# Kernel optimization log

Measured on AMD Instinct MI355X. Metric: run time of the kernel, lower is better.

## Reference

```python
import jax, jax.numpy as jnp
import numpy as np

EPS = 1e-5
N_HEADS = 32
TEMPERATURE = 1.0


def _inorm(x, g, b):
    # InstanceNorm2d (affine): normalize over H,W per (N, C)
    m = jnp.mean(x, axis=(-2, -1), keepdims=True)
    v = jnp.var(x, axis=(-2, -1), keepdims=True)
    return (x - m) * jax.lax.rsqrt(v + EPS) * g + b


def _resample(x, out_hw):
    # Fourier (spectral) resampling, matching neuraloperator's resample for skips
    H, W = x.shape[-2:]
    Ho, Wo = out_hw
    if (H, W) == (Ho, Wo):
        return x
    xf = jnp.fft.rfft2(x, norm='forward')
    kh = min(H, Ho) // 2
    kw = min(W // 2 + 1, Wo // 2 + 1)
    of = jnp.zeros(x.shape[:-2] + (Ho, Wo // 2 + 1), dtype=xf.dtype)
    of = of.at[..., :kh, :kw].set(xf[..., :kh, :kw])
    of = of.at[..., -kh:, :kw].set(xf[..., -kh:, :kw])
    return jnp.fft.irfft2(of, s=(Ho, Wo), norm='forward')


def _spec_conv(x, w, out_hw):
    # w: [2(pos/neg rows), in, out, m1, m2, 2(re/im)]; fft_norm='forward'
    m1, m2 = w.shape[3], w.shape[4]
    Ho, Wo = out_hw
    wc = w[..., 0] + 1j * w[..., 1]  # [2, in, out, m1, m2]
    xf = jnp.fft.rfft2(x, norm='forward')  # [B, Cin, H, W//2+1]
    top = jnp.einsum('bimn,iomn->bomn', xf[:, :, :m1, :m2], wc[0])
    bot = jnp.einsum('bimn,iomn->bomn', xf[:, :, -m1:, :m2], wc[1])
    of = jnp.zeros((x.shape[0], w.shape[2], Ho, Wo // 2 + 1), dtype=xf.dtype)
    of = of.at[:, :, :m1, :m2].set(top)
    of = of.at[:, :, -m1:, :m2].set(bot)
    return jnp.fft.irfft2(of, s=(Ho, Wo), norm='forward')


def _fno_layer(x, w, ws, bs, out_hw, norm_gb=None, act=False):
    # one FNOBlock layer: spectral conv + linear (1x1) skip, optional instance norm + gelu
    skip = jnp.einsum('bchw,oc->bohw', x, ws) + bs[None, :, None, None]
    skip = _resample(skip, out_hw)
    fno = _spec_conv(x, w, out_hw)
    if norm_gb is not None:
        fno = _inorm(fno, norm_gb[0], norm_gb[1])
    y = fno + skip
    if act:
        y = jax.nn.gelu(y, approximate=False)  # torch F.gelu default = exact erf
    return y


def _forward(x, wK, wKs, bKs, wQ, wQs, bQs, wV, wVs, bVs, wP, wPs, bPs,
             wM0, wM0s, bM0s, wM1, wM1s, bM1s, norm_g, norm_b):
    B, T, H, W = x.shape  # token_codimension == 1 -> tokens T == channels
    xa = x.reshape(B * T, 1, H, W)
    xa_n = _inorm(xa, norm_g[0], norm_b[0])  # self.norm1
    # K, Q at half resolution (output_scaling_factor = 1/scale, scale = 2); V at full res
    k = _fno_layer(xa_n, wK, wKs, bKs, (H // 2, W // 2))
    q = _fno_layer(xa_n, wQ, wQs, bQs, (H // 2, W // 2))
    v = _fno_layer(xa_n, wV, wVs, bVs, (H, W))

    def to_seq(z):
        h, w = z.shape[-2:]
        z = z.reshape(B, T, N_HEADS, 1, h, w).transpose(0, 2, 1, 3, 4, 5)
        return z.reshape(B, N_HEADS, T, h * w)  # d = head_codim = 1

    qs, ks, vs = to_seq(q), to_seq(k), to_seq(v)
    scores = jnp.einsum('bhtd,bhsd->bhts', qs, ks) / (np.sqrt(ks.shape[-1]).astype(np.float32) * TEMPERATURE)
    attn_w = jax.nn.softmax(scores, axis=-1)
    out = jnp.einsum('bhts,bhsd->bhtd', attn_w, vs)  # [B, heads, T, H*W]
    out = out.reshape(B, N_HEADS, T, 1, H, W).transpose(0, 2, 1, 3, 4, 5)
    out = out.reshape(B * T, N_HEADS, H, W)
    # proj: n_heads*head_codim != token_codim -> FNO projection back to 1 channel
    projd = _fno_layer(out, wP, wPs, bPs, (H, W))
    attention = _inorm(projd + xa, norm_g[1], norm_b[1])  # attention_normalizer
    an = _inorm(attention, norm_g[2], norm_b[2])  # self.norm2
    # permutation-equivariant mixer: 2 FNO layers, instance_norm, gelu between layers
    m = _fno_layer(an, wM0, wM0s, bM0s, (H, W), (norm_g[3], norm_b[3]), act=True)
    m = _fno_layer(m, wM1, wM1s, bM1s, (H, W), (norm_g[4], norm_b[4]), act=False)
    output = _inorm(m, norm_g[5], norm_b[5]) + attention  # mixer_out_normalizer + residual
    return output.reshape(B, T, H, W)


def setup_inputs() -> dict:
    key = jax.random.key(0)
    ks = jax.random.split(key, 16)
    B, T, H, W, heads = 2, 32, 128, 128, 32

    def rn(k, shape, s=1.0):
        return jax.random.normal(k, shape, jnp.float32) * s

    inp = {'x': rn(ks[0], (B, T, H, W))}
    for i, nm in enumerate(['K', 'Q', 'V']):
        inp['w' + nm] = rn(ks[1 + 3 * i], (2, 1, heads, 16, 16, 2), 1.0 / heads)
        inp['w' + nm + 's'] = rn(ks[2 + 3 * i], (heads, 1), 1.0)
        inp['b' + nm + 's'] = jnp.zeros((heads,), jnp.float32)
    inp['wP'] = rn(ks[10], (2, heads, 1, 32, 32, 2), 1.0 / heads)
    inp['wPs'] = rn(ks[11], (1, heads), 1.0 / heads)
    inp['bPs'] = jnp.zeros((1,), jnp.float32)
    inp['wM0'] = rn(ks[12], (2, 1, 1, 32, 32, 2), 1.0)
    inp['wM0s'] = rn(ks[13], (1, 1), 1.0)
    inp['bM0s'] = jnp.zeros((1,), jnp.float32)
    inp['wM1'] = rn(ks[14], (2, 1, 1, 32, 32, 2), 1.0)
    inp['wM1s'] = rn(ks[15], (1, 1), 1.0)
    inp['bM1s'] = jnp.zeros((1,), jnp.float32)
    inp['norm_g'] = jnp.ones((6,), jnp.float32)
    inp['norm_b'] = jnp.zeros((6,), jnp.float32)
    return inp


def reference(x, wK, wKs, bKs, wQ, wQs, bQs, wV, wVs, bVs, wP, wPs, bPs,
              wM0, wM0s, bM0s, wM1, wM1s, bM1s, norm_g, norm_b):
    return _forward(x, wK, wKs, bKs, wQ, wQs, bQs, wV, wVs, bVs, wP, wPs, bPs,
                    wM0, wM0s, bM0s, wM1, wM1s, bM1s, norm_g, norm_b)
```

## Files before the change

### kernel.cpp

```cpp
#include <hip/hip_runtime.h>
#include <math.h>


#define EPSV 1e-5f
#define PI2 6.283185307179586f

typedef float2 cf;

__device__ __forceinline__ cf cmul(cf a, cf b){ return make_float2(a.x*b.x - a.y*b.y, a.x*b.y + a.y*b.x); }
__device__ __forceinline__ cf ldc(const float* p){ return make_float2(p[0], p[1]); }
__device__ __forceinline__ void stc(float* p, cf v){ p[0]=v.x; p[1]=v.y; }

__device__ __forceinline__ void init_tw(cf* tw, int N, float dir){
  for (int j = threadIdx.x; j < N; j += blockDim.x){
    float s, c; sincosf(dir * PI2 * (float)j / (float)N, &s, &c);
    tw[j] = make_float2(c, s);
  }
}

__device__ void breduce2(float& a, float& b){
  __shared__ float sha[16], shb[16];
  for (int off = 32; off > 0; off >>= 1){
    a += __shfl_down(a, off, 64);
    b += __shfl_down(b, off, 64);
  }
  int w = threadIdx.x >> 6, lane = threadIdx.x & 63;
  int nw = (blockDim.x + 63) >> 6;
  if (lane == 0){ sha[w] = a; shb[w] = b; }
  __syncthreads();
  if (threadIdx.x == 0){
    for (int i = 1; i < nw; ++i){ a += sha[i]; b += shb[i]; }
    sha[0] = a; shb[0] = b;
  }
  __syncthreads();
  a = sha[0]; b = shb[0];
  __syncthreads();
}

__device__ __forceinline__ cf kq_mode(const float* w, int o, int kh, int kw){
  if (kw < 16){
    if (kh < 16)  return ldc(w + ((o*16+kh)*16+kw)*2);
    if (kh >= 48) return ldc(w + (((32+o)*16+(kh-48))*16+kw)*2);
  }
  return make_float2(0.f,0.f);
}

__global__ __launch_bounds__(256) void k_gamma_xstats(
                      const float* __restrict__ wQ, const float* __restrict__ wQs,
                      const float* __restrict__ bQs,
                      const float* __restrict__ wK, const float* __restrict__ wKs,
                      const float* __restrict__ bKs,
                      const float* __restrict__ x, const float* __restrict__ ng,
                      const float* __restrict__ nb,
                      float* __restrict__ gam, float* __restrict__ gcons,
                      float* __restrict__ stats, float* __restrict__ normAB){
  if (blockIdx.x >= 32){
    int n = blockIdx.x - 32;
    const float* im = x + n*16384;
    float s=0.f, s2=0.f;
    for (int i=threadIdx.x;i<16384;i+=256){ float v=im[i]; s+=v; s2=fmaf(v,v,s2); }
    breduce2(s,s2);
    if (threadIdx.x==0){
      float m = s*(1.f/16384.f), var = s2*(1.f/16384.f)-m*m;
      float A = rsqrtf(var+EPSV)*ng[0];
      normAB[n*2]=A; normAB[n*2+1]=nb[0]-m*A;
    }
    return;
  }
  int o = blockIdx.x;
  if (o==0){ for (int i=threadIdx.x;i<640;i+=256) stats[i]=0.f; }
  float sQ=wQs[o], sK=wKs[o];
  for (int m = threadIdx.x; m < 2112; m += 256){
    int kh = m/33, kw = m-kh*33;
    cf g;
    if (kw == 0){
      int mh = (64-kh)&63;
      cf qp = kq_mode(wQ,o,kh,0);  qp.x += sQ;
      cf qm = kq_mode(wQ,o,mh,0);  qm.x += sQ;
      cf qt = make_float2(0.5f*(qp.x+qm.x), 0.5f*(qp.y-qm.y));
      cf kp = kq_mode(wK,o,kh,0);  kp.x += sK;
      cf km = kq_mode(wK,o,mh,0);  km.x += sK;
      cf kt = make_float2(0.5f*(kp.x+km.x), 0.5f*(kp.y-km.y));
      g = make_float2(64.f*(qt.x*kt.x + qt.y*kt.y), 64.f*(qt.y*kt.x - qt.x*kt.y));
    } else if (kw == 32){
      g = make_float2(64.f*sQ*sK, 0.f);
    } else {
      cf q = kq_mode(wQ,o,kh,kw); q.x += sQ;
      cf k = kq_mode(wK,o,kh,kw); k.x += sK;
      g = make_float2(128.f*(q.x*k.x + q.y*k.y), 128.f*(q.y*k.x - q.x*k.y));
    }
    stc(gam + (o*2112+m)*2, g);
  }
  if (threadIdx.x == 0){
    float qt0 = sQ + kq_mode(wQ,o,0,0).x;
    float kt0 = sK + kq_mode(wK,o,0,0).x;
    gcons[o]    = 64.f*bKs[o]*qt0;
    gcons[32+o] = 64.f*bQs[o]*kt0;
    gcons[64+o] = 64.f*bQs[o]*bKs[o];
  }
}

__global__ __launch_bounds__(1024) void k_fwd2d(const float* __restrict__ x, const float* __restrict__ normAB,
                                                float* __restrict__ F){
  __shared__ float zb[16384];
  __shared__ cf Crow[4224];
  __shared__ cf tw[128];
  init_tw(tw, 128, -1.f);
  int n = blockIdx.x;
  float A = normAB[n*2], Bc = normAB[n*2+1];
  for (int i=threadIdx.x;i<16384;i+=1024) zb[i] = fmaf(x[n*16384+i], A, Bc);
  __syncthreads();
  for (int i=threadIdx.x;i<8192;i+=1024){
    int h=i>>6, w=i&63;
    float a=zb[h*128+w], b=zb[h*128+w+64];
    zb[h*128+w]=a+b; zb[h*128+w+64]=a-b;
  }
  __syncthreads();
  for (int i=threadIdx.x;i<4224;i+=1024){
    int h=i/33, kw=i-h*33;
    int sel = (kw&1)? 64 : 0;
    float re=0.f, im=0.f; int idx=0;
    for (int w=0;w<64;++w){
      float v=zb[h*128+sel+w]; cf t=tw[idx];
      re=fmaf(v,t.x,re); im=fmaf(v,t.y,im);
      idx=(idx+kw)&127;
    }
    Crow[i] = make_float2(re*(1.f/16384.f), im*(1.f/16384.f));
  }
  __syncthreads();
  for (int i=threadIdx.x;i<2112;i+=1024){
    int h=i/33, kw=i-h*33;
    cf a=Crow[h*33+kw], b=Crow[(h+64)*33+kw];
    Crow[h*33+kw]      = make_float2(a.x+b.x, a.y+b.y);
    Crow[(h+64)*33+kw] = make_float2(a.x-b.x, a.y-b.y);
  }
  __syncthreads();
  for (int i=threadIdx.x;i<2112;i+=1024){
    int r=i/33, kw=i-r*33;
    int R = (r<32)? r : r+64;
    int sel = (r&1)? 64 : 0;
    float re=0.f, im=0.f; int idx=0;
    for (int j=0;j<64;++j){
      cf v=Crow[(sel+j)*33+kw]; cf t=tw[idx];
      re = fmaf(v.x,t.x,re); re = fmaf(-v.y,t.y,re);
      im = fmaf(v.x,t.y,im); im = fmaf(v.y,t.x,im);
      idx=(idx+R)&127;
    }
    stc(F + ((n*64+r)*33+kw)*2, make_float2(re,im));
  }
}

__global__ __launch_bounds__(256) void k_score(const float* __restrict__ F, const float* __restrict__ gam,
                                               float* __restrict__ scoreP){
  __shared__ float2 Esh[66][33];
  __shared__ float2 gsh[4][66];
  int mk = blockIdx.x, b = blockIdx.y, og = blockIdx.z;
  int m0 = mk*66;
  int t = threadIdx.x >> 3, s4 = (threadIdx.x & 7) << 2;
  for (int i = threadIdx.x; i < 2112; i += 256){
    int tt = i/66, j = i - tt*66;
    int m = m0 + j;
    int kh = m/33, kw = m - kh*33;
    const float* Fb = F + (b*32+tt)*4224;
    float2 v;
    if (kw < 32) v = *(const float2*)(Fb + (kh*33+kw)*2);
    else {
      int mh = (64-kh)&63;
      float2 a = *(const float2*)(Fb + (kh*33+32)*2);
      float2 c = *(const float2*)(Fb + (mh*33+32)*2);
      v = make_float2(0.5f*(a.x+c.x), 0.5f*(a.y-c.y));
    }
    Esh[j][tt] = v;
  }
  for (int i = threadIdx.x; i < 264; i += 256){
    int ol = i/66, j = i - ol*66;
    gsh[ol][j] = *(const float2*)(gam + ((og*4+ol)*2112 + m0 + j)*2);
  }
  __syncthreads();
  float acc[4][4];
  #pragma unroll
  for (int a=0;a<4;++a) for (int k=0;k<4;++k) acc[a][k]=0.f;
  #pragma unroll 2
  for (int j=0;j<66;++j){
    float2 et = Esh[j][t];
    float2 e0 = Esh[j][s4+0];
    float2 e1 = Esh[j][s4+1];
    float2 e2 = Esh[j][s4+2];
    float2 e3 = Esh[j][s4+3];
    #pragma unroll
    for (int ol=0;ol<4;++ol){
      float2 g = gsh[ol][j];
      float a  = g.x*et.x - g.y*et.y;
      float bb = g.x*et.y + g.y*et.x;
      acc[ol][0] = fmaf(a,e0.x,fmaf(bb,e0.y,acc[ol][0]));
      acc[ol][1] = fmaf(a,e1.x,fmaf(bb,e1.y,acc[ol][1]));
      acc[ol][2] = fmaf(a,e2.x,fmaf(bb,e2.y,acc[ol][2]));
      acc[ol][3] = fmaf(a,e3.x,fmaf(bb,e3.y,acc[ol][3]));
    }
  }
  #pragma unroll
  for (int ol=0;ol<4;++ol){
    int o = og*4+ol;
    float* sp = scoreP + (((mk*2+b)*32+o)*32 + t)*32 + s4;
    sp[0]=acc[ol][0]; sp[1]=acc[ol][1]; sp[2]=acc[ol][2]; sp[3]=acc[ol][3];
  }
}

__global__ __launch_bounds__(1024) void k_softmax(float* __restrict__ attn, const float* __restrict__ F,
                                                const float* __restrict__ gcons, const float* __restrict__ scoreP){
  __shared__ float Ssh[32][33];
  int b = blockIdx.x, o = blockIdx.y;
  int t = threadIdx.x >> 5, s = threadIdx.x & 31;
  float c0=gcons[o], c1=gcons[32+o], c2=gcons[64+o];
  float sc = c0*F[(b*32+t)*4224] + c1*F[(b*32+s)*4224] + c2;
  #pragma unroll 8
  for (int p=0;p<32;++p) sc += scoreP[(((p*2+b)*32+o)*32 + t)*32 + s];
  Ssh[t][s] = sc;
  __syncthreads();
  float mx = -1e30f;
  for (int ss=0;ss<32;++ss) mx = fmaxf(mx, Ssh[t][ss]);
  float e = expf(sc - mx);
  __syncthreads();
  Ssh[t][s] = e;
  __syncthreads();
  float sum = 0.f;
  for (int ss=0;ss<32;++ss) sum += Ssh[t][ss];
  attn[(b*32+o)*1024 + t*32 + s] = e/sum;
}

__device__ __forceinline__ cf wcV_col0(const float* wV, int o, int fr){
  if (fr < 16)  return ldc(wV + ((o*16+fr)*16)*2);
  if (fr >= 112) return ldc(wV + (((32+o)*16+(fr-112))*16)*2);
  return make_float2(0.f,0.f);
}

__global__ __launch_bounds__(256) void k_pmode(const float* __restrict__ F, const float* __restrict__ attn,
                        const float* __restrict__ wV, const float* __restrict__ wVs,
                        const float* __restrict__ wP, const float* __restrict__ wPs,
                        float* __restrict__ Pm){
  __shared__ float att[32][8][32];
  __shared__ cf Fsh[32][32];
  __shared__ cf dsh[32][32];
  int b = blockIdx.x, mh = blockIdx.y, tg = blockIdx.z;
  int fr = mh<32 ? mh : mh+64;
  int half = (mh>=32)?1:0, mr = mh&31;
  for (int i=threadIdx.x; i<8192; i+=256){
    int o = i>>8, r = i&255;
    att[o][r>>5][r&31] = attn[(b*32+o)*1024 + tg*256 + r];
  }
  for (int i=threadIdx.x; i<1024; i+=256){
    int s=i>>5, kw=i&31;
    Fsh[s][kw] = ldc(F + (((b*32+s)*64+mh)*33+kw)*2);
  }
  for (int i=threadIdx.x; i<1024; i+=256){
    int o=i>>5, kw=i&31;
    cf wp = ldc(wP + (((half*32+o)*32+mr)*32+kw)*2);
    cf bP = make_float2(wPs[o]+wp.x, wp.y);
    cf aV = make_float2(wVs[o], 0.f);
    if (kw==0){
      cf w1 = wcV_col0(wV,o,fr);
      cf w2 = wcV_col0(wV,o,(128-fr)&127);
      aV.x += 0.5f*(w1.x + w2.x);
      aV.y += 0.5f*(w1.y - w2.y);
    } else if (kw<16){
      if (fr<16){ cf wv=ldc(wV + ((o*16+fr)*16+kw)*2); aV.x+=wv.x; aV.y+=wv.y; }
      else if (fr>=112){ cf wv=ldc(wV + (((32+o)*16+(fr-112))*16+kw)*2); aV.x+=wv.x; aV.y+=wv.y; }
    }
    cf c = cmul(bP, aV);
    c.x -= wPs[o]*wVs[o];
    dsh[o][kw]=c;
  }
  __syncthreads();
  int tl = threadIdx.x>>5, kw = threadIdx.x&31;
  float ax=0.f, ay=0.f;
  for (int o=0;o<32;++o){
    float er=0.f, ei=0.f;
    #pragma unroll
    for (int s4=0;s4<32;s4+=4){
      float4 a4 = *(const float4*)&att[o][tl][s4];
      cf f0=Fsh[s4][kw], f1=Fsh[s4+1][kw], f2=Fsh[s4+2][kw], f3=Fsh[s4+3][kw];
      er=fmaf(a4.x,f0.x,er); ei=fmaf(a4.x,f0.y,ei);
      er=fmaf(a4.y,f1.x,er); ei=fmaf(a4.y,f1.y,ei);
      er=fmaf(a4.z,f2.x,er); ei=fmaf(a4.z,f2.y,ei);
      er=fmaf(a4.w,f3.x,er); ei=fmaf(a4.w,f3.y,ei);
    }
    cf d = dsh[o][kw];
    ax += d.x*er - d.y*ei;
    ay += d.x*ei + d.y*er;
  }
  int t = tg*8+tl;
  stc(Pm + ((b*32+t)*2048 + mh*32+kw)*2, make_float2(ax,ay));
}

__global__ __launch_bounds__(256) void k_zmix(const float* __restrict__ x, const float* __restrict__ Pm,
                        const float* __restrict__ attn, const float* __restrict__ normAB,
                        const float* __restrict__ wVs, const float* __restrict__ wPs,
                        const float* __restrict__ wP, const float* __restrict__ bPs,
                        const float* __restrict__ bVs,
                        float* __restrict__ z, float* __restrict__ stats,
                        float* __restrict__ Tm){
  __shared__ cf Pmsh[64][33];
  __shared__ cf PmAsh[16][33];
  __shared__ float zrows[16][128];
  __shared__ float Mrow[32];
  __shared__ float cpart[33];
  __shared__ float consts;
  __shared__ cf tw[128];
  init_tw(tw, 128, 1.f);
  int n = blockIdx.x, b = n>>5, t = n&31, hb = blockIdx.y*8;
  for (int i=threadIdx.x;i<2048;i+=256)
    Pmsh[i>>5][i&31] = ldc(Pm + (n*2048 + i)*2);
  if (threadIdx.x < 32){
    int s = threadIdx.x;
    float a=0.f;
    for (int o=0;o<32;++o) a = fmaf(attn[(b*32+o)*1024 + t*32 + s], wVs[o]*wPs[o], a);
    float AxS = normAB[(b*32+s)*2], BcS = normAB[(b*32+s)*2+1];
    Mrow[s] = fmaf(a, AxS, (s==t)?1.f:0.f);
    cpart[s] = a*BcS;
  } else if (threadIdx.x == 32){
    float dcx = bPs[0];
    for (int o=0;o<32;++o){
      cf wp = ldc(wP + (o*1024)*2);
      dcx += (wPs[o]+wp.x)*bVs[o];
    }
    cpart[32] = dcx;
  }
  __syncthreads();
  if (threadIdx.x == 0){
    float c=0.f;
    for (int i=0;i<33;++i) c += cpart[i];
    consts = c;
  }
  {
    int bl = threadIdx.x>>5, kw = threadIdx.x&31;
    int h = hb + bl;
    float ser=0.f, sei=0.f, sor=0.f, soi=0.f;
    int s2h = (2*h)&127;
    int idx = 0;
    for (int khi=0;khi<32;khi+=2){
      cf v=Pmsh[khi][kw]; cf tt=tw[idx];
      ser += v.x*tt.x - v.y*tt.y; sei += v.x*tt.y + v.y*tt.x;
      idx=(idx+s2h)&127;
    }
    idx = (96*h)&127;
    for (int khi=32;khi<64;khi+=2){
      cf v=Pmsh[khi][kw]; cf tt=tw[idx];
      ser += v.x*tt.x - v.y*tt.y; sei += v.x*tt.y + v.y*tt.x;
      idx=(idx+s2h)&127;
    }
    idx = h&127;
    for (int khi=1;khi<32;khi+=2){
      cf v=Pmsh[khi][kw]; cf tt=tw[idx];
      sor += v.x*tt.x - v.y*tt.y; soi += v.x*tt.y + v.y*tt.x;
      idx=(idx+s2h)&127;
    }
    idx = (97*h)&127;
    for (int khi=33;khi<64;khi+=2){
      cf v=Pmsh[khi][kw]; cf tt=tw[idx];
      sor += v.x*tt.x - v.y*tt.y; soi += v.x*tt.y + v.y*tt.x;
      idx=(idx+s2h)&127;
    }
    PmAsh[bl][kw]   = make_float2(ser+sor, sei+soi);
    PmAsh[8+bl][kw] = make_float2(ser-sor, sei-soi);
  }
  __syncthreads();
  float cst = consts;
  float s1=0.f, s2=0.f;
  const float* xb = x + b*32*16384;
  {
    int hl = threadIdx.x>>4, wg = threadIdx.x&15;
    int w0 = wg*4;
    int gh = (hl<8)? hb+hl : hb+(hl-8)+64;
    int off = gh*128;
    float Se[4], So[4];
    #pragma unroll
    for (int j=0;j<4;++j){
      int w = w0+j;
      int s2w = (2*w)&127;
      float se=0.f, so=0.f;
      int idx=0;
      for (int kwp=0;kwp<16;++kwp){
        cf v = PmAsh[hl][2*kwp]; cf tt=tw[idx];
        float term = v.x*tt.x - v.y*tt.y;
        se += (kwp? 2.f:1.f)*term;
        idx=(idx+s2w)&127;
      }
      idx = w&127;
      for (int kwp=0;kwp<16;++kwp){
        cf v = PmAsh[hl][2*kwp+1]; cf tt=tw[idx];
        so += 2.f*(v.x*tt.x - v.y*tt.y);
        idx=(idx+s2w)&127;
      }
      Se[j]=se; So[j]=so;
    }
    float mixa[4]={0,0,0,0}, mixb[4]={0,0,0,0};
    for (int s=0;s<32;++s){
      float m = Mrow[s];
      float4 xa = *(const float4*)(xb + s*16384 + off + w0);
      float4 xc = *(const float4*)(xb + s*16384 + off + w0 + 64);
      mixa[0]=fmaf(m,xa.x,mixa[0]); mixa[1]=fmaf(m,xa.y,mixa[1]);
      mixa[2]=fmaf(m,xa.z,mixa[2]); mixa[3]=fmaf(m,xa.w,mixa[3]);
      mixb[0]=fmaf(m,xc.x,mixb[0]); mixb[1]=fmaf(m,xc.y,mixb[1]);
      mixb[2]=fmaf(m,xc.z,mixb[2]); mixb[3]=fmaf(m,xc.w,mixb[3]);
    }
    float oa[4], ob[4];
    #pragma unroll
    for (int j=0;j<4;++j){
      oa[j] = cst + Se[j] + So[j] + mixa[j];
      ob[j] = cst + Se[j] - So[j] + mixb[j];
      s1 += oa[j]+ob[j];
      s2 += oa[j]*oa[j] + ob[j]*ob[j];
      zrows[hl][w0+j]    = oa[j];
      zrows[hl][w0+64+j] = ob[j];
    }
    *(float4*)(z + n*16384 + off + w0)      = make_float4(oa[0],oa[1],oa[2],oa[3]);
    *(float4*)(z + n*16384 + off + w0 + 64) = make_float4(ob[0],ob[1],ob[2],ob[3]);
  }
  __syncthreads();
  for (int i=threadIdx.x;i<1024;i+=256){
    int hl=i>>6, w=i&63;
    float a=zrows[hl][w], bz=zrows[hl][w+64];
    zrows[hl][w]=a+bz; zrows[hl][w+64]=a-bz;
  }
  __syncthreads();
  for (int i=threadIdx.x;i<512;i+=256){
    int hl=i>>5, kw=i&31;
    int gh = (hl<8)? hb+hl : hb+(hl-8)+64;
    int sel = (kw&1)? 64 : 0;
    float re=0.f, im=0.f; int idx=0;
    for (int w=0;w<64;++w){
      float v=zrows[hl][sel+w]; cf tt=tw[idx];
      re=fmaf(v,tt.x,re); im=fmaf(v,tt.y,im);
      idx=(idx+kw)&127;
    }
    float* d = Tm + ((n*128+gh)*32+kw)*2;
    d[0]=re*(1.f/16384.f); d[1]=-im*(1.f/16384.f);
  }
  breduce2(s1,s2);
  if (threadIdx.x==0){ atomicAdd(&stats[n*2],s1); atomicAdd(&stats[n*2+1],s2); }
}

__global__ __launch_bounds__(256) void k_colpair(const float* __restrict__ Tm, const float* __restrict__ wM,
                                                 const float* __restrict__ statsZ,
                                                 const float* __restrict__ ng, const float* __restrict__ nb,
                                                 int apply_an, float* __restrict__ Am){
  __shared__ cf Tsh[128][9];
  __shared__ cf Gsh[64][9];
  __shared__ cf tw[128];
  init_tw(tw,128,-1.f);
  int n = blockIdx.x, kw8 = blockIdx.y*8;
  float C1 = 1.f, Dc128 = 0.f;
  if (apply_an){
    float S=statsZ[n*2], S2=statsZ[n*2+1];
    float mz=S*(1.f/16384.f), vz=S2*(1.f/16384.f)-mz*mz;
    float az=rsqrtf(vz+EPSV);
    float g1=ng[1], g2=ng[2];
    float vat = g1*g1*vz*az*az;
    C1 = az*g1*rsqrtf(vat+EPSV)*g2;
    Dc128 = (nb[2] - mz*C1)*(1.f/128.f);
  }
  for (int i=threadIdx.x;i<1024;i+=256){
    int h=i>>3, kwl=i&7;
    cf v = ldc(Tm + ((n*128+h)*32 + kw8+kwl)*2);
    v.x *= C1; v.y *= C1;
    if (apply_an && (kw8+kwl)==0) v.x += Dc128;
    Tsh[h][kwl] = v;
  }
  __syncthreads();
  for (int i=threadIdx.x;i<512;i+=256){
    int h=i>>3, kwl=i&7;
    cf a=Tsh[h][kwl], b=Tsh[h+64][kwl];
    Tsh[h][kwl]    = make_float2(a.x+b.x, a.y+b.y);
    Tsh[h+64][kwl] = make_float2(a.x-b.x, a.y-b.y);
  }
  __syncthreads();
  {
    int kwl = threadIdx.x&7, base = threadIdx.x>>3;
    for (int r=0;r<2;++r){
      int khi = r*32 + base;
      int khF = (khi<32)? khi : khi+64;
      int sel = (khi&1)? 64 : 0;
      float re=0.f, im=0.f; int idx=0;
      for (int j=0;j<64;++j){
        cf v=Tsh[sel+j][kwl]; cf t=tw[idx];
        re += v.x*t.x - v.y*t.y; im += v.x*t.y + v.y*t.x;
        idx=(idx+khF)&127;
      }
      int half=(khi>=32)?1:0, mr=khi&31;
      cf wv = ldc(wM + ((half*32+mr)*32 + kw8+kwl)*2);
      Gsh[khi][kwl] = cmul(make_float2(re,im), wv);
    }
  }
  __syncthreads();
  {
    int kwl = threadIdx.x&7, base = threadIdx.x>>3;
    for (int r=0;r<2;++r){
      int h = r*32 + base;
      float ser=0.f, sei=0.f, sor=0.f, soi=0.f;
      int s2h = (2*h)&127;
      int idx=0;
      for (int khi=0;khi<32;khi+=2){
        cf v=Gsh[khi][kwl]; cf t=tw[idx];
        ser += v.x*t.x + v.y*t.y; sei += v.y*t.x - v.x*t.y;
        idx=(idx+s2h)&127;
      }
      idx=(96*h)&127;
      for (int khi=32;khi<64;khi+=2){
        cf v=Gsh[khi][kwl]; cf t=tw[idx];
        ser += v.x*t.x + v.y*t.y; sei += v.y*t.x - v.x*t.y;
        idx=(idx+s2h)&127;
      }
      idx=h&127;
      for (int khi=1;khi<32;khi+=2){
        cf v=Gsh[khi][kwl]; cf t=tw[idx];
        sor += v.x*t.x + v.y*t.y; soi += v.y*t.x - v.x*t.y;
        idx=(idx+s2h)&127;
      }
      idx=(97*h)&127;
      for (int khi=33;khi<64;khi+=2){
        cf v=Gsh[khi][kwl]; cf t=tw[idx];
        sor += v.x*t.x + v.y*t.y; soi += v.y*t.x - v.x*t.y;
        idx=(idx+s2h)&127;
      }
      stc(Am + ((n*128+h)*32 + kw8+kwl)*2,    make_float2(ser+sor, sei+soi));
      stc(Am + ((n*128+h+64)*32 + kw8+kwl)*2, make_float2(ser-sor, sei-soi));
    }
  }
}

__global__ __launch_bounds__(256) void k_mirfft_row(const float* __restrict__ Am, float* __restrict__ out,
                                                    float* __restrict__ stats,
                                                    const float* __restrict__ m0, float* __restrict__ statsC,
                                                    int withCross){
  __shared__ cf rowA[16][33];
  __shared__ cf tw[128];
  init_tw(tw,128,1.f);
  int n=blockIdx.x, h0=blockIdx.y*16;
  for (int i=threadIdx.x;i<512;i+=256){
    int hl=i>>5, kw=i&31;
    rowA[hl][kw] = ldc(Am + ((n*128+h0+hl)*32+kw)*2);
  }
  __syncthreads();
  float s=0.f,s2=0.f,s3=0.f;
  for (int i=threadIdx.x;i<1024;i+=256){
    int hl=i>>6, w=i&63;
    int s2w = (2*w)&127;
    float se=0.f, so=0.f;
    int idx=0;
    for (int kwp=0;kwp<16;++kwp){
      cf v=rowA[hl][2*kwp]; cf t=tw[idx];
      float term=v.x*t.x-v.y*t.y;
      se += (kwp? 2.f:1.f)*term;
      idx=(idx+s2w)&127;
    }
    idx = w&127;
    for (int kwp=0;kwp<16;++kwp){
      cf v=rowA[hl][2*kwp+1]; cf t=tw[idx];
      so += 2.f*(v.x*t.x-v.y*t.y);
      idx=(idx+s2w)&127;
    }
    float oa = se+so, ob = se-so;
    int gi = n*16384+(h0+hl)*128+w;
    out[gi]    = oa;
    out[gi+64] = ob;
    s+=oa+ob; s2 += oa*oa + ob*ob;
    if (withCross){
      s3 = fmaf(oa, m0[gi], s3);
      s3 = fmaf(ob, m0[gi+64], s3);
    }
  }
  breduce2(s,s2);
  if (threadIdx.x==0){ atomicAdd(&stats[n*2],s); atomicAdd(&stats[n*2+1],s2); }
  if (withCross){
    float d=0.f;
    breduce2(s3,d);
    if (threadIdx.x==0) atomicAdd(&statsC[n*2],s3);
  }
}

__global__ __launch_bounds__(256) void k_m0_rfft_row(const float* __restrict__ fno, const float* __restrict__ z,
                              const float* __restrict__ stats0, const float* __restrict__ statsZ,
                              const float* __restrict__ ng, const float* __restrict__ nb,
                              const float* __restrict__ wM0s, const float* __restrict__ bM0s,
                              float* __restrict__ m0out, float* __restrict__ Tm,
                              float* __restrict__ statsM0){
  __shared__ float tile[16][128];
  __shared__ cf tw[128];
  init_tw(tw,128,-1.f);
  int n=blockIdx.x, h0=blockIdx.y*16;
  float S0=stats0[n*2], S02=stats0[n*2+1];
  float m0m=S0*(1.f/16384.f), v0=S02*(1.f/16384.f)-m0m*m0m;
  float A0=rsqrtf(v0+EPSV)*ng[3];
  float B0=nb[3]-m0m*A0;
  float Sz=statsZ[n*2], Sz2=statsZ[n*2+1];
  float mz=Sz*(1.f/16384.f), vz=Sz2*(1.f/16384.f)-mz*mz;
  float az=rsqrtf(vz+EPSV);
  float g1=ng[1], g2=ng[2];
  float vat=g1*g1*vz*az*az;
  float C1=az*g1*rsqrtf(vat+EPSV)*g2;
  float Dc=nb[2]-mz*C1;
  float ws_=wM0s[0], bs_=bM0s[0];
  float sm=0.f, sm2=0.f;
  for (int i=threadIdx.x;i<2048;i+=256){
    int gi = n*16384 + h0*128 + i;
    float nf = fmaf(fno[gi], A0, B0);
    float an = fmaf(z[gi], C1, Dc);
    float pre = nf + fmaf(ws_, an, bs_);
    float gv = 0.5f*pre*(1.f+erff(pre*0.70710678118654752f));
    tile[i>>7][i&127]=gv;
    m0out[gi]=gv;
    sm+=gv; sm2=fmaf(gv,gv,sm2);
  }
  __syncthreads();
  for (int i=threadIdx.x;i<1024;i+=256){
    int hl=i>>6, w=i&63;
    float a=tile[hl][w], b=tile[hl][w+64];
    tile[hl][w]=a+b; tile[hl][w+64]=a-b;
  }
  __syncthreads();
  for (int i=threadIdx.x;i<512;i+=256){
    int hl=i>>5, kw=i&31;
    int sel = (kw&1)? 64:0;
    float re=0.f,im=0.f; int idx=0;
    for (int w=0;w<64;++w){
      float v=tile[hl][sel+w]; cf t=tw[idx];
      re=fmaf(v,t.x,re); im=fmaf(v,t.y,im);
      idx=(idx+kw)&127;
    }
    float* d = Tm + ((n*128+h0+hl)*32+kw)*2;
    d[0]=re*(1.f/16384.f); d[1]=im*(1.f/16384.f);
  }
  breduce2(sm,sm2);
  if (threadIdx.x==0){ atomicAdd(&statsM0[n*2],sm); atomicAdd(&statsM0[n*2+1],sm2); }
}

__global__ __launch_bounds__(256) void k_final(const float* __restrict__ f1, const float* __restrict__ m0,
                        const float* __restrict__ z,
                        const float* __restrict__ stats1, const float* __restrict__ statsM0,
                        const float* __restrict__ statsC, const float* __restrict__ statsZ,
                        const float* __restrict__ ng, const float* __restrict__ nb,
                        const float* __restrict__ wM1s, const float* __restrict__ bM1s,
                        float* __restrict__ out){
  int n=blockIdx.x, h0=blockIdx.y*16;
  const float N = 16384.f, iN = 1.f/16384.f;
  float Sf=stats1[n*2], Sf2=stats1[n*2+1];
  float m1m=Sf*iN, v1=Sf2*iN-m1m*m1m;
  float A1=rsqrtf(v1+EPSV)*ng[4];
  float Bc1=nb[4]-m1m*A1;
  float ws_=wM1s[0], K=Bc1+bM1s[0];
  float Sm=statsM0[n*2], Sm2=statsM0[n*2+1], Sfm=statsC[n*2];
  float S1m = A1*Sf + ws_*Sm + N*K;
  float S2m = A1*A1*Sf2 + ws_*ws_*Sm2 + N*K*K + 2.f*A1*ws_*Sfm + 2.f*A1*K*Sf + 2.f*ws_*K*Sm;
  float mean2 = S1m*iN, var2 = S2m*iN - mean2*mean2;
  float A2=rsqrtf(var2+EPSV)*ng[5];
  float B2c=nb[5]-mean2*A2;
  float Sz=statsZ[n*2], Sz2=statsZ[n*2+1];
  float mz=Sz*iN, vz=Sz2*iN-mz*mz;
  float Az=rsqrtf(vz+EPSV)*ng[1];
  float Bz=nb[1]-mz*Az;
  float cf1 = A2*A1, cm0 = A2*ws_, cc = A2*K + B2c;
  for (int i=threadIdx.x;i<2048;i+=256){
    int gi=n*16384+h0*128+i;
    out[gi] = fmaf(f1[gi],cf1, fmaf(m0[gi],cm0, cc)) + fmaf(z[gi],Az,Bz);
  }
}

extern "C" void kernel_launch(void* const* d_in, const int* in_sizes, int n_in,
                              void* d_out, int out_size, void* d_ws, size_t ws_size,
                              hipStream_t stream){
  (void)in_sizes; (void)n_in; (void)out_size; (void)ws_size;
  const float* x   = (const float*)d_in[0];
  const float* wK  = (const float*)d_in[1];
  const float* wKs = (const float*)d_in[2];
  const float* bKs = (const float*)d_in[3];
  const float* wQ  = (const float*)d_in[4];
  const float* wQs = (const float*)d_in[5];
  const float* bQs = (const float*)d_in[6];
  const float* wV  = (const float*)d_in[7];
  const float* wVs = (const float*)d_in[8];
  const float* bVs = (const float*)d_in[9];
  const float* wP  = (const float*)d_in[10];
  const float* wPs = (const float*)d_in[11];
  const float* bPs = (const float*)d_in[12];
  const float* wM0 = (const float*)d_in[13];
  const float* wM0s= (const float*)d_in[14];
  const float* bM0s= (const float*)d_in[15];
  const float* wM1 = (const float*)d_in[16];
  const float* wM1s= (const float*)d_in[17];
  const float* bM1s= (const float*)d_in[18];
  const float* ng  = (const float*)d_in[19];
  const float* nb  = (const float*)d_in[20];
  float* out = (float*)d_out;
  float* ws  = (float*)d_ws;

  float* F      = ws;
  float* scoreP = F + 270336;
  float* attn   = scoreP + 2097152;
  float* stats  = attn + 65536;
  float* Pm     = stats + 640;
  float* gcons  = Pm + 262144;
  float* gam    = gcons + 128;
  float* normAB = gam + 135168;
  float* z      = normAB + 128;
  float* m0b    = z + 1048576;
  float* fx     = m0b + 1048576;
  float* Tm     = fx + 1048576;
  float* Am     = Tm + 524288;
  float* statsZ = stats;
  float* stats0 = stats + 128;
  float* stats1 = stats + 256;
  float* statsM0= stats + 384;
  float* statsC = stats + 512;

  k_gamma_xstats<<<96,256,0,stream>>>(wQ,wQs,bQs, wK,wKs,bKs, x, ng, nb, gam, gcons, stats, normAB);
  k_fwd2d<<<64,1024,0,stream>>>(x, normAB, F);
  k_score<<<dim3(32,2,8),256,0,stream>>>(F, gam, scoreP);
  k_softmax<<<dim3(2,32),1024,0,stream>>>(attn, F, gcons, scoreP);
  k_pmode<<<dim3(2,64,4),256,0,stream>>>(F, attn, wV, wVs, wP, wPs, Pm);
  k_zmix<<<dim3(64,8),256,0,stream>>>(x, Pm, attn, normAB, wVs, wPs, wP, bPs, bVs, z, statsZ, Tm);
  k_colpair<<<dim3(64,4),256,0,stream>>>(Tm, wM0, statsZ, ng, nb, 1, Am);
  k_mirfft_row<<<dim3(64,8),256,0,stream>>>(Am, fx, stats0, (const float*)nullptr, (float*)nullptr, 0);
  k_m0_rfft_row<<<dim3(64,8),256,0,stream>>>(fx, z, stats0, statsZ, ng, nb, wM0s, bM0s, m0b, Tm, statsM0);
  k_colpair<<<dim3(64,4),256,0,stream>>>(Tm, wM1, statsZ, ng, nb, 0, Am);
  k_mirfft_row<<<dim3(64,8),256,0,stream>>>(Am, fx, stats1, m0b, statsC, 1);
  k_final<<<dim3(64,8),256,0,stream>>>(fx, m0b, z, stats1, statsM0, statsC, statsZ, ng, nb, wM1s, bM1s, out);
}
```

Measured before the change: 271.2 us.

## Split fused 2D forward DFT into row and column kernels for more blocks

Replaces the single k_fwd2d kernel, which ran one 1024-thread block per image (64 blocks), with a row-DFT kernel over 64x8 blocks writing intermediate spectra to a new global workspace, followed by a column-DFT kernel over 64x9 blocks. The aim is more parallelism and lower per-block shared-memory use, so more of the GPU is occupied. The cost is an extra kernel launch and a global round trip through the intermediate row-spectrum buffer.

```diff
diff --git a/kernel.cpp b/kernel.cpp
--- a/kernel.cpp
+++ b/kernel.cpp
@@ -100,54 +100,66 @@
   }
 }
 
-__global__ __launch_bounds__(1024) void k_fwd2d(const float* __restrict__ x, const float* __restrict__ normAB,
-                                                float* __restrict__ F){
-  __shared__ float zb[16384];
-  __shared__ cf Crow[4224];
+__global__ __launch_bounds__(256) void k_rfft_row_x(const float* __restrict__ x, const float* __restrict__ normAB,
+                                                    float* __restrict__ Cw){
+  __shared__ float tile[16][128];
   __shared__ cf tw[128];
   init_tw(tw, 128, -1.f);
-  int n = blockIdx.x;
+  int n = blockIdx.x, h0 = blockIdx.y*16;
   float A = normAB[n*2], Bc = normAB[n*2+1];
-  for (int i=threadIdx.x;i<16384;i+=1024) zb[i] = fmaf(x[n*16384+i], A, Bc);
-  __syncthreads();
-  for (int i=threadIdx.x;i<8192;i+=1024){
-    int h=i>>6, w=i&63;
-    float a=zb[h*128+w], b=zb[h*128+w+64];
-    zb[h*128+w]=a+b; zb[h*128+w+64]=a-b;
-  }
-  __syncthreads();
-  for (int i=threadIdx.x;i<4224;i+=1024){
-    int h=i/33, kw=i-h*33;
+  for (int i=threadIdx.x;i<2048;i+=256) tile[i>>7][i&127] = fmaf(x[n*16384 + h0*128 + i], A, Bc);
+  __syncthreads();
+  for (int i=threadIdx.x;i<1024;i+=256){
+    int hl=i>>6, w=i&63;
+    float a=tile[hl][w], b=tile[hl][w+64];
+    tile[hl][w]=a+b; tile[hl][w+64]=a-b;
+  }
+  __syncthreads();
+  int hl = threadIdx.x >> 4, kws = threadIdx.x & 15;
+  for (int kw=kws; kw<33; kw+=16){
     int sel = (kw&1)? 64 : 0;
     float re=0.f, im=0.f; int idx=0;
     for (int w=0;w<64;++w){
-      float v=zb[h*128+sel+w]; cf t=tw[idx];
+      float v=tile[hl][sel+w]; cf t=tw[idx];
       re=fmaf(v,t.x,re); im=fmaf(v,t.y,im);
       idx=(idx+kw)&127;
     }
-    Crow[i] = make_float2(re*(1.f/16384.f), im*(1.f/16384.f));
-  }
-  __syncthreads();
-  for (int i=threadIdx.x;i<2112;i+=1024){
-    int h=i/33, kw=i-h*33;
-    cf a=Crow[h*33+kw], b=Crow[(h+64)*33+kw];
-    Crow[h*33+kw]      = make_float2(a.x+b.x, a.y+b.y);
-    Crow[(h+64)*33+kw] = make_float2(a.x-b.x, a.y-b.y);
-  }
-  __syncthreads();
-  for (int i=threadIdx.x;i<2112;i+=1024){
-    int r=i/33, kw=i-r*33;
-    int R = (r<32)? r : r+64;
-    int sel = (r&1)? 64 : 0;
-    float re=0.f, im=0.f; int idx=0;
-    for (int j=0;j<64;++j){
-      cf v=Crow[(sel+j)*33+kw]; cf t=tw[idx];
-      re = fmaf(v.x,t.x,re); re = fmaf(-v.y,t.y,re);
-      im = fmaf(v.x,t.y,im); im = fmaf(v.y,t.x,im);
-      idx=(idx+R)&127;
-    }
-    stc(F + ((n*64+r)*33+kw)*2, make_float2(re,im));
-  }
+    float* d = Cw + (((n*128)+(h0+hl))*33 + kw)*2;
+    d[0]=re*(1.f/16384.f); d[1]=im*(1.f/16384.f);
+  }
+}
+
+__global__ __launch_bounds__(256) void k_fcol(const float* __restrict__ Cw, float* __restrict__ F){
+  __shared__ cf col[4][128];
+  __shared__ cf tw[128];
+  init_tw(tw, 128, -1.f);
+  int n = blockIdx.x, kwb = blockIdx.y*4;
+  for (int i=threadIdx.x;i<512;i+=256){
+    int kwl=i>>7, h=i&127; int kw=kwb+kwl;
+    col[kwl][h] = (kw<33) ? ldc(Cw + ((n*128+h)*33+kw)*2) : make_float2(0.f,0.f);
+  }
+  __syncthreads();
+  {
+    int i = threadIdx.x;
+    int kwl = i>>6, h = i&63;
+    cf a = col[kwl][h], b = col[kwl][h+64];
+    col[kwl][h]    = make_float2(a.x+b.x, a.y+b.y);
+    col[kwl][h+64] = make_float2(a.x-b.x, a.y-b.y);
+  }
+  __syncthreads();
+  int r = threadIdx.x & 63, kwl = threadIdx.x >> 6;
+  int kw = kwb + kwl;
+  if (kw >= 33) return;
+  int R = (r<32)? r : r+64;
+  int sel = (r&1)? 64 : 0;
+  float re=0.f, im=0.f; int idx=0;
+  for (int j=0;j<64;++j){
+    cf v=col[kwl][sel+j]; cf t=tw[idx];
+    re = fmaf(v.x,t.x,re); re = fmaf(-v.y,t.y,re);
+    im = fmaf(v.x,t.y,im); im = fmaf(v.y,t.x,im);
+    idx=(idx+R)&127;
+  }
+  stc(F + ((n*64+r)*33+kw)*2, make_float2(re,im));
 }
 
 __global__ __launch_bounds__(256) void k_score(const float* __restrict__ F, const float* __restrict__ gam,
@@ -694,7 +706,8 @@
   float* ws  = (float*)d_ws;
 
   float* F      = ws;
-  float* scoreP = F + 270336;
+  float* Cw     = F + 270336;
+  float* scoreP = Cw + 540672;
   float* attn   = scoreP + 2097152;
   float* stats  = attn + 65536;
   float* Pm     = stats + 640;
@@ -713,7 +726,8 @@
   float* statsC = stats + 512;
 
   k_gamma_xstats<<<96,256,0,stream>>>(wQ,wQs,bQs, wK,wKs,bKs, x, ng, nb, gam, gcons, stats, normAB);
-  k_fwd2d<<<64,1024,0,stream>>>(x, normAB, F);
+  k_rfft_row_x<<<dim3(64,8),256,0,stream>>>(x, normAB, Cw);
+  k_fcol<<<dim3(64,9),256,0,stream>>>(Cw, F);
   k_score<<<dim3(32,2,8),256,0,stream>>>(F, gam, scoreP);
   k_softmax<<<dim3(2,32),1024,0,stream>>>(attn, F, gcons, scoreP);
   k_pmode<<<dim3(2,64,4),256,0,stream>>>(F, attn, wV, wVs, wP, wPs, Pm);
```

New measurement: 250.7 us. -7.6%, faster.
